# Kernel tuning notes

Measured on AMD Instinct MI355X. Metric: run time of the kernel, lower is better.

The kernel has to match this reference:

```python
import jax, jax.numpy as jnp
import numpy as np

N, D, C, K, M = 32768, 512, 64, 16, 128
DEPTH = 4            # log2(K): decision-tree depth per codebook
NODES = K - 1        # 15 internal tree nodes per codebook


def _build_selection_matrix():
    # Node i of the binary tree lives at level log2(i+1) and thresholds the
    # level-l selected dimension of its codebook.
    S = np.zeros((C * NODES, C * DEPTH), dtype=np.float32)
    base = np.zeros((NODES, DEPTH), dtype=np.float32)
    for i in range(NODES):
        base[i, int(np.log2(i + 1))] = 1.0
    for c in range(C):
        S[c * NODES:(c + 1) * NODES, c * DEPTH:(c + 1) * DEPTH] = base
    return S


def _build_bit_matrix():
    # Leaf k scores +1/-1 on each of its DEPTH ancestor nodes; the true leaf
    # attains the maximal score DEPTH.
    base = np.zeros((K, NODES), dtype=np.float32)
    for k in range(K):
        for l in range(DEPTH):
            node = (1 << l) - 1 + (k >> (DEPTH - l))   # ancestor at level l
            bit = (k >> (DEPTH - 1 - l)) & 1            # right(1)/left(0)
            base[k, node] = 1.0 if bit else -1.0
    B = np.zeros((C * K, C * NODES), dtype=np.float32)
    for c in range(C):
        B[c * K:(c + 1) * K, c * NODES:(c + 1) * NODES] = base
    return B


def setup_inputs() -> dict:
    key = jax.random.key(0)
    k1, k2, k3, k4 = jax.random.split(key, 4)
    I = jax.random.normal(k1, (N, D), jnp.float32)
    T = jax.random.normal(k2, (C * NODES,), jnp.float32) * 0.1   # thresholds
    L = jax.random.normal(k3, (M, C, K), jnp.float32)            # LUT
    dims = jnp.sort(jax.random.randint(k4, (C * DEPTH,), 0, D))  # selected cols
    S = jnp.asarray(_build_selection_matrix())
    B = jnp.asarray(_build_bit_matrix())
    temp = jnp.ones((1,), jnp.float32)
    return {"I": I, "T": T, "L": L, "S": S, "B": B, "dims": dims, "temp": temp}


def reference(I, T, L, S, B, dims, temp):
    t = temp[0]
    x_sel = I[:, dims]                                  # (N, C*DEPTH) gather
    h = x_sel @ S.T - T                                 # (N, C*NODES)
    tanh_h = jnp.tanh(h / t)
    # straight-through sign: forward sign(h), backward d(tanh(h/t))
    sign_ste = jnp.sign(h) - jax.lax.stop_gradient(tanh_h) + tanh_h
    b = sign_ste @ B.T                                  # (N, C*K) leaf scores
    soft = jax.nn.softmax(b.reshape(-1, C, K) / t, axis=2)
    hard = jax.nn.one_hot(jnp.argmax(soft, axis=2), K, dtype=soft.dtype)
    # straight-through one-hot encoding E: forward hard, backward soft
    E = hard - jax.lax.stop_gradient(soft) + soft       # (N, C, K)
    return jnp.einsum("nck,mck->nm", E, L)              # LUT gather-sum readout
```

## Files before the change

### kernel.cpp

```cpp
#include <hip/hip_runtime.h>

#define N_TOTAL 32768
#define D_DIM   512
#define C_DIM   64
#define K_DIM   16
#define M_DIM   128
#define NODES_  15

typedef unsigned short u16;
typedef unsigned int   u32;
typedef unsigned long long u64;
typedef unsigned char  u8;
typedef float  f32x4  __attribute__((ext_vector_type(4)));
typedef short  short8v __attribute__((ext_vector_type(8)));

__device__ __forceinline__ u32 f2bf_bits(float f) {
    u32 u = __float_as_uint(f);
    return (u + 0x7FFFu + ((u >> 16) & 1u)) >> 16;
}

__device__ __forceinline__ void gload_lds4(const float* g, float* l) {
    __builtin_amdgcn_global_load_lds(
        (const __attribute__((address_space(1))) void*)g,
        (__attribute__((address_space(3))) void*)l, 4, 0, 0);
}

__global__ __launch_bounds__(256) void build_lb(
    const float* __restrict__ L, u16* __restrict__ Lb)
{
    int i0 = (blockIdx.x * 256 + threadIdx.x) * 8;
    float4 a = *(const float4*)(L + i0);
    float4 b = *(const float4*)(L + i0 + 4);
    u32 w0 = f2bf_bits(a.x) | (f2bf_bits(a.y) << 16);
    u32 w1 = f2bf_bits(a.z) | (f2bf_bits(a.w) << 16);
    u32 w2 = f2bf_bits(b.x) | (f2bf_bits(b.y) << 16);
    u32 w3 = f2bf_bits(b.z) | (f2bf_bits(b.w) << 16);
    *(uint4*)(Lb + i0) = make_uint4(w0, w1, w2, w3);
}

__global__ __launch_bounds__(256) void codes_kernel(
    const float* __restrict__ I,
    const float* __restrict__ T,
    const int* __restrict__ dims,
    u8* __restrict__ cws)
{
    __shared__ float sIg[16 * 256];
    __shared__ float sT[C_DIM * NODES_];

    const int tid  = threadIdx.x;
    const int lane = tid & 63;
    const int wv   = tid >> 6;
    const int rowBase = blockIdx.x * 16 + wv * 4;

    int dlv[4];
    #pragma unroll
    for (int i = 0; i < 4; ++i) dlv[i] = dims[i * 64 + lane];

    #pragma unroll
    for (int rr = 0; rr < 4; ++rr) {
        const float* src = I + (size_t)(rowBase + rr) * D_DIM;
        float* dst = sIg + (wv * 4 + rr) * 256;
        #pragma unroll
        for (int i = 0; i < 4; ++i)
            gload_lds4(src + dlv[i], dst + i * 64);
    }

    for (int j = tid; j < C_DIM * NODES_; j += 256) sT[j] = T[j];
    __syncthreads();

    const float* tc = sT + lane * NODES_;
    u32 cp = 0;
    #pragma unroll
    for (int rr = 0; rr < 4; ++rr) {
        const float4 x = *(const float4*)(sIg + (wv * 4 + rr) * 256 + lane * 4);
        int node = 0, k = 0;
        int b0 = (x.x - tc[0] > 0.0f) ? 1 : 0;
        k = b0; node = 1 + b0;
        int b1 = (x.y - tc[node] > 0.0f) ? 1 : 0;
        k = (k << 1) | b1; node = (node << 1) + 1 + b1;
        int b2 = (x.z - tc[node] > 0.0f) ? 1 : 0;
        k = (k << 1) | b2; node = (node << 1) + 1 + b2;
        int b3 = (x.w - tc[node] > 0.0f) ? 1 : 0;
        k = (k << 1) | b3;
        cp |= (u32)k << (4 * rr);
    }

    u32 cw =  (cp & 0xFu)
           | ((cp >> 4)  & 0xFu) << 8
           | ((cp >> 8)  & 0xFu) << 16
           | ((cp >> 12) & 0xFu) << 24;
    *(u32*)(cws + (size_t)lane * N_TOTAL + rowBase) = cw;
}

__global__ __launch_bounds__(256) void gemm_kernel(
    const u16* __restrict__ Lb,
    const u8* __restrict__ cws,
    float* __restrict__ out)
{
    __shared__ u8 sC[C_DIM * 64];

    const int tid  = threadIdx.x;
    const int lane = tid & 63;
    const int wv   = tid >> 6;
    const int rowBase = blockIdx.x * 64;

    {
        int cls = tid >> 2, off = (tid & 3) * 16;
        *(uint4*)(sC + cls * 64 + off) =
            *(const uint4*)(cws + (size_t)cls * N_TOTAL + rowBase + off);
    }
    __syncthreads();

    const int l15     = lane & 15;
    const int clsLane = (lane >> 5) & 1;
    const int kb      = ((lane >> 4) & 1) * 8;

    f32x4 acc[4][2] = {};

    const u16* lb0 = Lb + (size_t)((wv * 2 + 0) * 16 + l15) * 1024 + ((lane >> 4) * 8);
    const u16* lb1 = Lb + (size_t)((wv * 2 + 1) * 16 + l15) * 1024 + ((lane >> 4) * 8);

    #pragma unroll 4
    for (int ch = 0; ch < 32; ++ch) {
        union { uint4 u; short8v v; } b0, b1;
        b0.u = *(const uint4*)(lb0 + ch * 32);
        b1.u = *(const uint4*)(lb1 + ch * 32);
        const int cls = ch * 2 + clsLane;
        #pragma unroll
        for (int rt = 0; rt < 4; ++rt) {
            u32 cd = sC[cls * 64 + rt * 16 + l15];
            u32 tt = cd - (u32)kb;
            u64 sv = 0x3F80ull << ((tt & 3) * 16);
            union { u64 d[2]; short8v v; } a;
            a.d[0] = (tt < 4) ? sv : 0ull;
            a.d[1] = (tt >= 4 && tt < 8) ? sv : 0ull;
            acc[rt][0] = __builtin_amdgcn_mfma_f32_16x16x32_bf16(
                             a.v, b0.v, acc[rt][0], 0, 0, 0);
            acc[rt][1] = __builtin_amdgcn_mfma_f32_16x16x32_bf16(
                             a.v, b1.v, acc[rt][1], 0, 0, 0);
        }
    }

    #pragma unroll
    for (int rt = 0; rt < 4; ++rt) {
        #pragma unroll
        for (int cj = 0; cj < 2; ++cj) {
            int col = (wv * 2 + cj) * 16 + l15;
            int r0  = rowBase + rt * 16 + ((lane >> 4) << 2);
            float* o = out + (size_t)r0 * M_DIM + col;
            o[0 * M_DIM] = acc[rt][cj][0];
            o[1 * M_DIM] = acc[rt][cj][1];
            o[2 * M_DIM] = acc[rt][cj][2];
            o[3 * M_DIM] = acc[rt][cj][3];
        }
    }
}

extern "C" void kernel_launch(void* const* d_in, const int* in_sizes, int n_in,
                              void* d_out, int out_size, void* d_ws, size_t ws_size,
                              hipStream_t stream) {
    const float* I    = (const float*)d_in[0];
    const float* T    = (const float*)d_in[1];
    const float* L    = (const float*)d_in[2];
    const int*   dims = (const int*)d_in[5];

    u16* Lb = (u16*)d_ws;
    u8*  cw = (u8*)d_ws + (1 << 18);

    hipLaunchKernelGGL(build_lb,   dim3(64),   dim3(256), 0, stream, L, Lb);
    hipLaunchKernelGGL(codes_kernel, dim3(N_TOTAL / 16), dim3(256), 0, stream,
                       I, T, dims, cw);
    hipLaunchKernelGGL(gemm_kernel, dim3(N_TOTAL / 64), dim3(256), 0, stream,
                       Lb, cw, (float*)d_out);
}
```

Before: 132.1 us.

## Load full input rows with 16-byte LDS DMA and pre-swizzle LUT into MFMA fragment order

The codes kernel now streams each row of I into LDS with contiguous 16-byte global_load_lds transfers and gathers the selected dims from shared memory, replacing the 4-byte scattered gather DMA. The LUT conversion kernel writes bf16 data already laid out in per-lane MFMA fragment order, so each wave's B loads in the GEMM are fully contiguous. The cost is reading all 512 columns of I instead of only the 256 selected ones, which roughly doubles DRAM traffic for the input while making every access coalesced.

```diff
diff --git a/kernel.cpp b/kernel.cpp
--- a/kernel.cpp
+++ b/kernel.cpp
@@ -6,6 +6,7 @@
 #define K_DIM   16
 #define M_DIM   128
 #define NODES_  15
+#define ROWS    16
 
 typedef unsigned short u16;
 typedef unsigned int   u32;
@@ -19,23 +20,29 @@
     return (u + 0x7FFFu + ((u >> 16) & 1u)) >> 16;
 }
 
-__device__ __forceinline__ void gload_lds4(const float* g, float* l) {
+__device__ __forceinline__ void gload_lds16(const float* g, float* l) {
     __builtin_amdgcn_global_load_lds(
         (const __attribute__((address_space(1))) void*)g,
-        (__attribute__((address_space(3))) void*)l, 4, 0, 0);
+        (__attribute__((address_space(3))) void*)l, 16, 0, 0);
 }
 
-__global__ __launch_bounds__(256) void build_lb(
-    const float* __restrict__ L, u16* __restrict__ Lb)
+__global__ __launch_bounds__(256) void build_lbf(
+    const float* __restrict__ L, u16* __restrict__ Lbf)
 {
-    int i0 = (blockIdx.x * 256 + threadIdx.x) * 8;
-    float4 a = *(const float4*)(L + i0);
-    float4 b = *(const float4*)(L + i0 + 4);
+    int idx  = blockIdx.x * 256 + threadIdx.x;
+    int lane = idx & 63;
+    int ch   = (idx >> 6) & 31;
+    int ct   = idx >> 11;
+    int m  = ct * 16 + (lane & 15);
+    int k0 = ch * 32 + ((lane >> 4) * 8);
+    const float* src = L + (size_t)m * 1024 + k0;
+    float4 a = *(const float4*)(src);
+    float4 b = *(const float4*)(src + 4);
     u32 w0 = f2bf_bits(a.x) | (f2bf_bits(a.y) << 16);
     u32 w1 = f2bf_bits(a.z) | (f2bf_bits(a.w) << 16);
     u32 w2 = f2bf_bits(b.x) | (f2bf_bits(b.y) << 16);
     u32 w3 = f2bf_bits(b.z) | (f2bf_bits(b.w) << 16);
-    *(uint4*)(Lb + i0) = make_uint4(w0, w1, w2, w3);
+    *(uint4*)(Lbf + (size_t)idx * 8) = make_uint4(w0, w1, w2, w3);
 }
 
 __global__ __launch_bounds__(256) void codes_kernel(
@@ -44,26 +51,23 @@
     const int* __restrict__ dims,
     u8* __restrict__ cws)
 {
-    __shared__ float sIg[16 * 256];
+    __shared__ float sI[ROWS * D_DIM];
     __shared__ float sT[C_DIM * NODES_];
 
     const int tid  = threadIdx.x;
     const int lane = tid & 63;
     const int wv   = tid >> 6;
-    const int rowBase = blockIdx.x * 16 + wv * 4;
+    const int rowBase = blockIdx.x * ROWS + wv * 4;
 
-    int dlv[4];
-    #pragma unroll
-    for (int i = 0; i < 4; ++i) dlv[i] = dims[i * 64 + lane];
+    {
+        const float* src = I + (size_t)rowBase * D_DIM;
+        float* dst = sI + wv * 4 * D_DIM;
+        #pragma unroll
+        for (int i = 0; i < 8; ++i)
+            gload_lds16(src + i * 256 + lane * 4, dst + i * 256);
+    }
 
-    #pragma unroll
-    for (int rr = 0; rr < 4; ++rr) {
-        const float* src = I + (size_t)(rowBase + rr) * D_DIM;
-        float* dst = sIg + (wv * 4 + rr) * 256;
-        #pragma unroll
-        for (int i = 0; i < 4; ++i)
-            gload_lds4(src + dlv[i], dst + i * 64);
-    }
+    const int4 dml = ((const int4*)dims)[lane];
 
     for (int j = tid; j < C_DIM * NODES_; j += 256) sT[j] = T[j];
     __syncthreads();
@@ -72,15 +76,16 @@
     u32 cp = 0;
     #pragma unroll
     for (int rr = 0; rr < 4; ++rr) {
-        const float4 x = *(const float4*)(sIg + (wv * 4 + rr) * 256 + lane * 4);
+        const float* v = sI + (wv * 4 + rr) * D_DIM;
+        float x0 = v[dml.x], x1 = v[dml.y], x2 = v[dml.z], x3 = v[dml.w];
         int node = 0, k = 0;
-        int b0 = (x.x - tc[0] > 0.0f) ? 1 : 0;
+        int b0 = (x0 - tc[0] > 0.0f) ? 1 : 0;
         k = b0; node = 1 + b0;
-        int b1 = (x.y - tc[node] > 0.0f) ? 1 : 0;
+        int b1 = (x1 - tc[node] > 0.0f) ? 1 : 0;
         k = (k << 1) | b1; node = (node << 1) + 1 + b1;
-        int b2 = (x.z - tc[node] > 0.0f) ? 1 : 0;
+        int b2 = (x2 - tc[node] > 0.0f) ? 1 : 0;
         k = (k << 1) | b2; node = (node << 1) + 1 + b2;
-        int b3 = (x.w - tc[node] > 0.0f) ? 1 : 0;
+        int b3 = (x3 - tc[node] > 0.0f) ? 1 : 0;
         k = (k << 1) | b3;
         cp |= (u32)k << (4 * rr);
     }
@@ -93,7 +98,7 @@
 }
 
 __global__ __launch_bounds__(256) void gemm_kernel(
-    const u16* __restrict__ Lb,
+    const u16* __restrict__ Lbf,
     const u8* __restrict__ cws,
     float* __restrict__ out)
 {
@@ -117,14 +122,14 @@
 
     f32x4 acc[4][2] = {};
 
-    const u16* lb0 = Lb + (size_t)((wv * 2 + 0) * 16 + l15) * 1024 + ((lane >> 4) * 8);
-    const u16* lb1 = Lb + (size_t)((wv * 2 + 1) * 16 + l15) * 1024 + ((lane >> 4) * 8);
+    const u16* lb0 = Lbf + ((size_t)(wv * 2 + 0) * 32 * 64 + lane) * 8;
+    const u16* lb1 = Lbf + ((size_t)(wv * 2 + 1) * 32 * 64 + lane) * 8;
 
     #pragma unroll 4
     for (int ch = 0; ch < 32; ++ch) {
         union { uint4 u; short8v v; } b0, b1;
-        b0.u = *(const uint4*)(lb0 + ch * 32);
-        b1.u = *(const uint4*)(lb1 + ch * 32);
+        b0.u = *(const uint4*)(lb0 + (size_t)ch * 64 * 8);
+        b1.u = *(const uint4*)(lb1 + (size_t)ch * 64 * 8);
         const int cls = ch * 2 + clsLane;
         #pragma unroll
         for (int rt = 0; rt < 4; ++rt) {
@@ -164,12 +169,12 @@
     const float* L    = (const float*)d_in[2];
     const int*   dims = (const int*)d_in[5];
 
-    u16* Lb = (u16*)d_ws;
-    u8*  cw = (u8*)d_ws + (1 << 18);
+    u16* Lbf = (u16*)d_ws;
+    u8*  cw  = (u8*)d_ws + (1 << 18);
 
-    hipLaunchKernelGGL(build_lb,   dim3(64),   dim3(256), 0, stream, L, Lb);
-    hipLaunchKernelGGL(codes_kernel, dim3(N_TOTAL / 16), dim3(256), 0, stream,
+    hipLaunchKernelGGL(build_lbf, dim3(64), dim3(256), 0, stream, L, Lbf);
+    hipLaunchKernelGGL(codes_kernel, dim3(N_TOTAL / ROWS), dim3(256), 0, stream,
                        I, T, dims, cw);
     hipLaunchKernelGGL(gemm_kernel, dim3(N_TOTAL / 64), dim3(256), 0, stream,
-                       Lb, cw, (float*)d_out);
+                       Lbf, cw, (float*)d_out);
 }
```

Measured after the change: 129.8 us. No clear change (-1.7%).
